# Optimization experiments

Hardware: AMD Instinct MI355X
Metric: run time of the kernel (lower is better)

Reference implementation:

```python
import math
import jax, jax.numpy as jnp
import numpy as np

K_NEIGH = 8  # module's self.k

def setup_inputs() -> dict:
    key = jax.random.key(0)
    ks = jax.random.split(key, 5)
    B, N, D = 4, 4096, 256
    s = 1.0 / math.sqrt(D)
    return {
        "x": jax.random.normal(ks[0], (B, N, D), dtype=jnp.float32),
        "Wqkv": jax.random.normal(ks[1], (3 * D, D), dtype=jnp.float32) * s,
        "bqkv": jax.random.normal(ks[2], (3 * D,), dtype=jnp.float32) * 0.02,
        "Wout": jax.random.normal(ks[3], (D, D), dtype=jnp.float32) * s,
        "bout": jax.random.normal(ks[4], (D,), dtype=jnp.float32) * 0.02,
    }

def reference(x, Wqkv, bqkv, Wout, bout):
    B, N, D = x.shape
    qkv = x @ Wqkv.T + bqkv                      # [B,N,3D]
    q, k, v = jnp.split(qkv, 3, axis=-1)         # each [B,N,D]
    # F.normalize(k, dim=-1) with eps=1e-12
    kn = k / jnp.maximum(jnp.linalg.norm(k, axis=-1, keepdims=True), 1e-12)
    sim = jnp.einsum('bnd,bmd->bnm', kn, kn)     # [B,N,N] cosine similarity
    sim = sim - 1e9 * jnp.eye(N, dtype=sim.dtype)
    k_val = min(K_NEIGH, N - 1)
    _, idx = jax.lax.top_k(sim, k_val)           # [B,N,k] neighbor indices
    # NOTE: the torch code builds k.unsqueeze(2).expand(B,N,N,D) and gathers on
    # dim 2, but that tensor is CONSTANT along dim 2, so the gather reduces to a
    # broadcast of k (and v) over the neighbor axis -- reproduced faithfully:
    k_sel = jnp.broadcast_to(k[:, :, None, :], (B, N, k_val, D))
    v_sel = jnp.broadcast_to(v[:, :, None, :], (B, N, k_val, D))
    scores = jnp.sum(q[:, :, None, :] * k_sel, axis=-1) / math.sqrt(D)  # [B,N,k]
    attn = jax.nn.softmax(scores, axis=-1)
    out = jnp.sum(attn[..., None] * v_sel, axis=2)                      # [B,N,D]
    return x + out @ Wout.T + bout
```

## Files before the change

kernel.cpp:

```cpp
#include <hip/hip_runtime.h>
#include <hip/hip_bf16.h>

#define DD 256
#define NROWS 16384

typedef float f32x4 __attribute__((ext_vector_type(4)));
typedef __bf16 bf16x4 __attribute__((ext_vector_type(4)));
typedef __bf16 bf16x8 __attribute__((ext_vector_type(8)));

__device__ __forceinline__ bf16x8 cvt8(f32x4 lo, f32x4 hi) {
  bf16x8 v;
#pragma unroll
  for (int j = 0; j < 4; ++j) {
    v[j] = (__bf16)lo[j];
    v[4 + j] = (__bf16)hi[j];
  }
  return v;
}

__global__ __launch_bounds__(1024) void wc_bc_kernel(
    const float* __restrict__ Wqkv, const float* __restrict__ bqkv,
    const float* __restrict__ Wout, const float* __restrict__ bout,
    __bf16* __restrict__ Wc, float* __restrict__ bc) {
  __shared__ float part[16][4][64];
  __shared__ float red[4];
  const int b = blockIdx.x;
  const int i0 = (b >> 2) * 4;
  const int qc = b & 3;
  const int c0 = qc * 64;
  const int t = threadIdx.x;
  const int w = t >> 6, l = t & 63;
  const float* __restrict__ Wv = Wqkv + 2 * DD * DD;
  const float* __restrict__ bv = bqkv + 2 * DD;

  float wo[4][16];
#pragma unroll
  for (int r = 0; r < 4; ++r)
#pragma unroll
    for (int jj = 0; jj < 16; ++jj)
      wo[r][jj] = Wout[(size_t)(i0 + r) * DD + w * 16 + jj];

  float acc0 = 0.f, acc1 = 0.f, acc2 = 0.f, acc3 = 0.f;
  const float* wvp = Wv + (size_t)(w * 16) * DD + c0 + l;
#pragma unroll
  for (int jj = 0; jj < 16; ++jj) {
    const float wv = wvp[(size_t)jj * DD];
    acc0 += wo[0][jj] * wv;
    acc1 += wo[1][jj] * wv;
    acc2 += wo[2][jj] * wv;
    acc3 += wo[3][jj] * wv;
  }
  part[w][0][l] = acc0;
  part[w][1][l] = acc1;
  part[w][2][l] = acc2;
  part[w][3][l] = acc3;

  if (qc == 0 && t < 256) {
    const int r = t >> 6, ll = t & 63;
    float p = 0.f;
#pragma unroll
    for (int k = 0; k < 4; ++k)
      p += Wout[(size_t)(i0 + r) * DD + k * 64 + ll] * bv[k * 64 + ll];
#pragma unroll
    for (int off = 32; off > 0; off >>= 1) p += __shfl_down(p, off);
    if (ll == 0) red[r] = p;
  }
  __syncthreads();
  if (t < 256) {
    const int r = t >> 6, ll = t & 63;
    float s = 0.f;
#pragma unroll
    for (int k = 0; k < 16; ++k) s += part[k][r][ll];
    Wc[(size_t)(i0 + r) * DD + c0 + ll] = (__bf16)s;
    if (qc == 0 && ll == 0) bc[i0 + r] = bout[i0 + r] + red[r];
  }
}

__global__ __launch_bounds__(1024, 2) void knn_attn_main(
    const float* __restrict__ x, const __bf16* __restrict__ Wc,
    const float* __restrict__ bc, float* __restrict__ out) {
  __shared__ __bf16 xs[32 * DD];

  const int t = threadIdx.x;
  const int w = t >> 6, l = t & 63;
  const int Rbase = blockIdx.x * 32;
  const int xrow = l & 15, g4 = l >> 4;
  const int C0 = w * 16;

  bf16x8 af[8];
  {
    const __bf16* wrp = Wc + (size_t)(C0 + xrow) * DD + g4 * 8;
#pragma unroll
    for (int ks = 0; ks < 8; ++ks) af[ks] = *(const bf16x8*)(wrp + ks * 32);
  }
  const f32x4 bias = *(const f32x4*)(bc + C0 + g4 * 4);

  {
    const int sr = t >> 5, sc = t & 31;
    const int ssw = (sr & 7) << 4;
    const float* s0 = x + (size_t)(Rbase + sr) * DD + sc * 8;
    f32x4 a = *(const f32x4*)(s0);
    f32x4 b = *(const f32x4*)(s0 + 4);
    *(bf16x8*)((char*)xs + ((sr * 512 + sc * 16) ^ ssw)) = cvt8(a, b);
  }
  __syncthreads();

#pragma unroll
  for (int rt = 0; rt < 2; ++rt) {
    const int lrow = rt * 16 + xrow;
    const int lsw = (lrow & 7) << 4;
    bf16x8 xf[8];
#pragma unroll
    for (int ks = 0; ks < 8; ++ks)
      xf[ks] = *(const bf16x8*)((const char*)xs +
                                ((lrow * 512 + ks * 64 + g4 * 16) ^ lsw));
    f32x4 acc = {0.f, 0.f, 0.f, 0.f};
#pragma unroll
    for (int ks = 0; ks < 8; ++ks)
      acc = __builtin_amdgcn_mfma_f32_16x16x32_bf16(af[ks], xf[ks], acc, 0, 0, 0);
    const int ocol = C0 + g4 * 4;
    bf16x4 xr4 = *(const bf16x4*)((const char*)xs +
                                  ((lrow * 512 + ocol * 2) ^ lsw));
    f32x4 xres;
#pragma unroll
    for (int j = 0; j < 4; ++j) xres[j] = (float)xr4[j];
    *(f32x4*)(out + (size_t)(Rbase + lrow) * DD + ocol) = acc + xres + bias;
  }
}

extern "C" void kernel_launch(void* const* d_in, const int* in_sizes, int n_in,
                              void* d_out, int out_size, void* d_ws, size_t ws_size,
                              hipStream_t stream) {
  const float* x = (const float*)d_in[0];
  const float* Wqkv = (const float*)d_in[1];
  const float* bqkv = (const float*)d_in[2];
  const float* Wout = (const float*)d_in[3];
  const float* bout = (const float*)d_in[4];
  float* out = (float*)d_out;

  __bf16* Wc = (__bf16*)d_ws;
  float* bc = (float*)((char*)d_ws + DD * DD * sizeof(__bf16));

  wc_bc_kernel<<<DD, 1024, 0, stream>>>(Wqkv, bqkv, Wout, bout, Wc, bc);
  knn_attn_main<<<NROWS / 32, 1024, 0, stream>>>(x, Wc, bc, out);
}
```

Measured before the change: 22.28 us.

## Retile main GEMM to 64 rows by 128 columns, stage output through LDS

Each block now handles 64 rows and half of the output columns, giving 512 blocks instead of 512 blocks of 32 rows by all columns. The output is staged in a swizzled LDS buffer and written back as row-contiguous nontemporal stores to coalesce global writes. Each x row tile is now loaded twice (once per column group), which adds input traffic. The larger LDS footprint (32KB x plus 32KB output) may reduce occupancy.

```diff
diff --git a/kernel.cpp b/kernel.cpp
--- a/kernel.cpp
+++ b/kernel.cpp
@@ -79,35 +79,45 @@
 __global__ __launch_bounds__(1024, 2) void knn_attn_main(
     const float* __restrict__ x, const __bf16* __restrict__ Wc,
     const float* __restrict__ bc, float* __restrict__ out) {
-  __shared__ __bf16 xs[32 * DD];
+  __shared__ __bf16 xs[64 * DD];
+  __shared__ float osd[64 * 128];
 
   const int t = threadIdx.x;
   const int w = t >> 6, l = t & 63;
-  const int Rbase = blockIdx.x * 32;
+  const int rb = blockIdx.x & 255;
+  const int cg = blockIdx.x >> 8;
+  const int Rbase = rb * 64;
+  const int C0blk = cg * 128;
+
   const int xrow = l & 15, g4 = l >> 4;
-  const int C0 = w * 16;
+  const int cg16 = w & 7;
+  const int rg = w >> 3;
 
   bf16x8 af[8];
   {
-    const __bf16* wrp = Wc + (size_t)(C0 + xrow) * DD + g4 * 8;
+    const __bf16* wrp = Wc + (size_t)(C0blk + cg16 * 16 + xrow) * DD + g4 * 8;
 #pragma unroll
     for (int ks = 0; ks < 8; ++ks) af[ks] = *(const bf16x8*)(wrp + ks * 32);
   }
-  const f32x4 bias = *(const f32x4*)(bc + C0 + g4 * 4);
+  const f32x4 bias = *(const f32x4*)(bc + C0blk + cg16 * 16 + g4 * 4);
 
   {
-    const int sr = t >> 5, sc = t & 31;
+    const int sr = t >> 4, sc = t & 15;
     const int ssw = (sr & 7) << 4;
-    const float* s0 = x + (size_t)(Rbase + sr) * DD + sc * 8;
-    f32x4 a = *(const f32x4*)(s0);
+    const int sbase = sr * 512 + sc * 32;
+    const float* s0 = x + (size_t)(Rbase + sr) * DD + sc * 16;
+    f32x4 a = *(const f32x4*)(s0 + 0);
     f32x4 b = *(const f32x4*)(s0 + 4);
-    *(bf16x8*)((char*)xs + ((sr * 512 + sc * 16) ^ ssw)) = cvt8(a, b);
+    f32x4 c = *(const f32x4*)(s0 + 8);
+    f32x4 d = *(const f32x4*)(s0 + 12);
+    *(bf16x8*)((char*)xs + ((sbase + 0) ^ ssw)) = cvt8(a, b);
+    *(bf16x8*)((char*)xs + ((sbase + 16) ^ ssw)) = cvt8(c, d);
   }
   __syncthreads();
 
 #pragma unroll
   for (int rt = 0; rt < 2; ++rt) {
-    const int lrow = rt * 16 + xrow;
+    const int lrow = rg * 32 + rt * 16 + xrow;
     const int lsw = (lrow & 7) << 4;
     bf16x8 xf[8];
 #pragma unroll
@@ -118,13 +128,26 @@
 #pragma unroll
     for (int ks = 0; ks < 8; ++ks)
       acc = __builtin_amdgcn_mfma_f32_16x16x32_bf16(af[ks], xf[ks], acc, 0, 0, 0);
-    const int ocol = C0 + g4 * 4;
+    const int ocol = C0blk + cg16 * 16 + g4 * 4;
+    const int oc_loc = cg16 * 64 + g4 * 16;
     bf16x4 xr4 = *(const bf16x4*)((const char*)xs +
                                   ((lrow * 512 + ocol * 2) ^ lsw));
     f32x4 xres;
 #pragma unroll
     for (int j = 0; j < 4; ++j) xres[j] = (float)xr4[j];
-    *(f32x4*)(out + (size_t)(Rbase + lrow) * DD + ocol) = acc + xres + bias;
+    f32x4 o = acc + xres + bias;
+    *(f32x4*)((char*)osd + (lrow * 512 + (oc_loc ^ lsw))) = o;
+  }
+  __syncthreads();
+
+#pragma unroll
+  for (int j = 0; j < 2; ++j) {
+    const int r = w * 4 + j * 2 + (l >> 5);
+    const int cbl = (l & 31) * 16;
+    const int cbp = cbl ^ ((r & 7) << 4);
+    f32x4 o = *(const f32x4*)((const char*)osd + (r * 512 + cbp));
+    __builtin_nontemporal_store(
+        o, (f32x4*)(out + (size_t)(Rbase + r) * DD + C0blk + (cbl >> 2)));
   }
 }
 
@@ -142,5 +165,5 @@
   float* bc = (float*)((char*)d_ws + DD * DD * sizeof(__bf16));
 
   wc_bc_kernel<<<DD, 1024, 0, stream>>>(Wqkv, bqkv, Wout, bout, Wc, bc);
-  knn_attn_main<<<NROWS / 32, 1024, 0, stream>>>(x, Wc, bc, out);
+  knn_attn_main<<<512, 1024, 0, stream>>>(x, Wc, bc, out);
 }
```

Result: no change. 22.62 us (+1.5%).

## Process 64 rows per block and stage output through LDS for coalesced nontemporal stores

Applied to the files above, without the earlier changes.

Each block now handles 64 rows instead of 32, which halves the grid and amortises the per-block load of Wc fragments. Output tiles are transposed through a double-buffered swizzled LDS buffer so that each wave writes one full contiguous row using nontemporal stores, replacing the scattered 16-byte column-strip stores. The cost is more LDS per block (96KB), a barrier per row tile, and fewer blocks to fill the GPU (256 blocks), which may limit occupancy.

```diff
diff --git a/kernel.cpp b/kernel.cpp
--- a/kernel.cpp
+++ b/kernel.cpp
@@ -79,11 +79,12 @@
 __global__ __launch_bounds__(1024, 2) void knn_attn_main(
     const float* __restrict__ x, const __bf16* __restrict__ Wc,
     const float* __restrict__ bc, float* __restrict__ out) {
-  __shared__ __bf16 xs[32 * DD];
+  __shared__ __bf16 xs[64 * DD];
+  __shared__ float osd[2][16 * DD];
 
   const int t = threadIdx.x;
   const int w = t >> 6, l = t & 63;
-  const int Rbase = blockIdx.x * 32;
+  const int Rblk = blockIdx.x * 64;
   const int xrow = l & 15, g4 = l >> 4;
   const int C0 = w * 16;
 
@@ -96,35 +97,59 @@
   const f32x4 bias = *(const f32x4*)(bc + C0 + g4 * 4);
 
   {
-    const int sr = t >> 5, sc = t & 31;
+    const int sr = t >> 4, sc = t & 15;
     const int ssw = (sr & 7) << 4;
-    const float* s0 = x + (size_t)(Rbase + sr) * DD + sc * 8;
-    f32x4 a = *(const f32x4*)(s0);
+    const int sbase = sr * 512 + sc * 32;
+    const float* s0 = x + (size_t)(Rblk + sr) * DD + sc * 16;
+    f32x4 a = *(const f32x4*)(s0 + 0);
     f32x4 b = *(const f32x4*)(s0 + 4);
-    *(bf16x8*)((char*)xs + ((sr * 512 + sc * 16) ^ ssw)) = cvt8(a, b);
+    f32x4 c = *(const f32x4*)(s0 + 8);
+    f32x4 d = *(const f32x4*)(s0 + 12);
+    *(bf16x8*)((char*)xs + ((sbase + 0) ^ ssw)) = cvt8(a, b);
+    *(bf16x8*)((char*)xs + ((sbase + 16) ^ ssw)) = cvt8(c, d);
   }
   __syncthreads();
 
+  const int ocol = C0 + g4 * 4;
+  const int xsw = (xrow & 7) << 4;
+
 #pragma unroll
-  for (int rt = 0; rt < 2; ++rt) {
-    const int lrow = rt * 16 + xrow;
-    const int lsw = (lrow & 7) << 4;
+  for (int i = 0; i < 4; ++i) {
+    const int lrow = i * 16 + xrow;
     bf16x8 xf[8];
 #pragma unroll
     for (int ks = 0; ks < 8; ++ks)
       xf[ks] = *(const bf16x8*)((const char*)xs +
-                                ((lrow * 512 + ks * 64 + g4 * 16) ^ lsw));
+                                ((lrow * 512 + ks * 64 + g4 * 16) ^ xsw));
     f32x4 acc = {0.f, 0.f, 0.f, 0.f};
 #pragma unroll
     for (int ks = 0; ks < 8; ++ks)
       acc = __builtin_amdgcn_mfma_f32_16x16x32_bf16(af[ks], xf[ks], acc, 0, 0, 0);
-    const int ocol = C0 + g4 * 4;
     bf16x4 xr4 = *(const bf16x4*)((const char*)xs +
-                                  ((lrow * 512 + ocol * 2) ^ lsw));
+                                  ((lrow * 512 + ocol * 2) ^ xsw));
     f32x4 xres;
 #pragma unroll
     for (int j = 0; j < 4; ++j) xres[j] = (float)xr4[j];
-    *(f32x4*)(out + (size_t)(Rbase + lrow) * DD + ocol) = acc + xres + bias;
+    f32x4 o = acc + xres + bias;
+    *(f32x4*)((char*)&osd[i & 1][0] + (xrow * 1024 + ((ocol * 4) ^ xsw))) = o;
+
+    if (i > 0) {
+      const int pr = (i - 1) * 16 + w;
+      const int cbp = (l * 16) ^ ((w & 7) << 4);
+      f32x4 ov = *(const f32x4*)((const char*)&osd[(i - 1) & 1][0] +
+                                 (w * 1024 + cbp));
+      __builtin_nontemporal_store(
+          ov, (f32x4*)(out + (size_t)(Rblk + pr) * DD + l * 4));
+    }
+    __syncthreads();
+  }
+
+  {
+    const int pr = 3 * 16 + w;
+    const int cbp = (l * 16) ^ ((w & 7) << 4);
+    f32x4 ov = *(const f32x4*)((const char*)&osd[1][0] + (w * 1024 + cbp));
+    __builtin_nontemporal_store(
+        ov, (f32x4*)(out + (size_t)(Rblk + pr) * DD + l * 4));
   }
 }
 
@@ -142,5 +167,5 @@
   float* bc = (float*)((char*)d_ws + DD * DD * sizeof(__bf16));
 
   wc_bc_kernel<<<DD, 1024, 0, stream>>>(Wqkv, bqkv, Wout, bout, Wc, bc);
-  knn_attn_main<<<NROWS / 32, 1024, 0, stream>>>(x, Wc, bc, out);
+  knn_attn_main<<<NROWS / 64, 1024, 0, stream>>>(x, Wc, bc, out);
 }
```

New measurement: 19.17 us. 14.0% less time.
